# Kernel tuning notes

Measured on AMD Instinct MI355X. Metric: run time of the kernel, lower is better.

The kernel has to match this reference:

```python
import jax, jax.numpy as jnp
import numpy as np

# Module config (matches init_kwargs)
B, H, W, C = 8, 32, 32, 512
NH = 8                      # num_heads
D = C // NH                 # per-head qkv channels (downsize_factor = num_heads)
HO = 512 // NH              # head_output_channels = output_channels // num_heads
COUT = 512                  # output_channels (== C so shortcut works)
EPS = 1e-3                  # keras BatchNormalization default epsilon


def setup_inputs() -> dict:
    key = jax.random.key(0)
    ks = jax.random.split(key, 10)
    s_in = C ** -0.5
    return {
        "x": jax.random.normal(ks[0], (B, H, W, C), jnp.float32),
        # 1x1 convs == per-head matmuls, no bias (use_bias=False)
        "Wk": jax.random.normal(ks[1], (NH, C, D), jnp.float32) * s_in,
        "Wq": jax.random.normal(ks[2], (NH, C, D), jnp.float32) * s_in,
        "Wv": jax.random.normal(ks[3], (NH, C, D), jnp.float32) * s_in,
        "Wo_head": jax.random.normal(ks[4], (NH, D, HO), jnp.float32) * (D ** -0.5),
        # per-head BatchNorm (inference: moving statistics)
        "gamma": jnp.ones((NH, HO), jnp.float32),
        "beta": jnp.zeros((NH, HO), jnp.float32),
        "mov_mean": jnp.zeros((NH, HO), jnp.float32),
        "mov_var": jnp.ones((NH, HO), jnp.float32),
        # relative position embeddings, init stddev = channels**-0.5
        "rel_w": jax.random.normal(ks[5], (NH, 2 * W - 1, D), jnp.float32) * s_in,
        "rel_h": jax.random.normal(ks[6], (NH, 2 * H - 1, D), jnp.float32) * s_in,
        # final 1x1 conv over concatenated heads
        "Wout": jax.random.normal(ks[7], (NH * HO, COUT), jnp.float32) * ((NH * HO) ** -0.5),
    }


def rel_to_abs(x):
    # x: [b, nh, L, 2L-1] relative logits -> [b, nh, L, L] absolute logits
    b, nh, L, _ = x.shape
    x = jnp.pad(x, ((0, 0), (0, 0), (0, 0), (0, 1)))        # [b,nh,L,2L]
    flat = x.reshape(b, nh, L * 2 * L)
    flat = jnp.pad(flat, ((0, 0), (0, 0), (0, L - 1)))       # [b,nh,2L^2+L-1]
    final = flat.reshape(b, nh, L + 1, 2 * L - 1)
    return final[:, :, :L, L - 1:]


def reference(x, Wk, Wq, Wv, Wo_head, gamma, beta, mov_mean, mov_var, rel_w, rel_h, Wout):
    b, h, w, c = x.shape
    n = h * w
    xf = x.reshape(b, n, c)
    # per-head 1x1 conv projections -> [b, nh, n, d]
    k = jnp.einsum('bnc,hcd->bhnd', xf, Wk)
    q = jnp.einsum('bnc,hcd->bhnd', xf, Wq)
    v = jnp.einsum('bnc,hcd->bhnd', xf, Wv)
    # Keras Dot(axes=2)([key, query]): rows index key positions, cols query positions
    scores = jnp.einsum('bhid,bhjd->bhij', k, q)             # [b,nh,n,n]
    # relative position logits computed from q (spatial mode)
    q5 = q.reshape(b, NH, h, w, D)
    wl = jnp.einsum('bhxyd,hmd->bhxym', q5, rel_w)           # [b,nh,H,W,2W-1]
    w_abs = rel_to_abs(wl.reshape(b * NH, h, w, 2 * w - 1)).reshape(b, NH, h, w, w)
    hl = jnp.einsum('bhxyd,hmd->bhyxm', q5, rel_h)           # [b,nh,W,H,2H-1] (q transposed x<->y)
    h_abs = rel_to_abs(hl.reshape(b * NH, w, h, 2 * h - 1)).reshape(b, NH, w, h, h)
    h_abs = h_abs.transpose(0, 1, 3, 2, 4)                   # [b,nh,x,y,x2]
    # logits[(x,y),(x2,y2)] = w_abs[x,y,y2] + h_abs[x,y,x2]
    s6 = scores.reshape(b, NH, h, w, h, w)
    s6 = s6 + w_abs[:, :, :, :, None, :] + h_abs[:, :, :, :, :, None]
    attn = jax.nn.softmax(s6.reshape(b, NH, n, n), axis=-1)
    out = jnp.einsum('bhij,bhjd->bhid', attn, v)             # [b,nh,n,d]
    ho = jnp.einsum('bhid,hde->bhie', out, Wo_head)          # per-head output 1x1 conv
    # per-head BatchNorm (inference)
    ho = gamma[None, :, None, :] * (ho - mov_mean[None, :, None, :]) * \
         jax.lax.rsqrt(mov_var[None, :, None, :] + EPS) + beta[None, :, None, :]
    cat = ho.transpose(0, 2, 1, 3).reshape(b, n, NH * HO)    # channel concat of heads
    y = (cat @ Wout).reshape(b, h, w, COUT)                  # final 1x1 conv
    return y + x                                             # shortcut connection
```

## Files before the change

### kernel.cpp

```cpp
#include <hip/hip_runtime.h>
#include <stdint.h>

typedef unsigned short u16;
typedef __attribute__((ext_vector_type(8))) short short8;
typedef __attribute__((ext_vector_type(4))) float f32x4;
typedef __attribute__((ext_vector_type(16))) float f32x16;
typedef __attribute__((ext_vector_type(4))) unsigned short us4;
typedef __attribute__((ext_vector_type(4))) uint32_t u32x4;
typedef __attribute__((ext_vector_type(2))) int i32x2;
typedef __attribute__((ext_vector_type(4))) int i32x4;

#define MFMA(a,b,c)   __builtin_amdgcn_mfma_f32_16x16x32_bf16((a),(b),(c),0,0,0)
#define MFMA32(a,b,c) __builtin_amdgcn_mfma_f32_32x32x16_bf16((a),(b),(c),0,0,0)
#define L2E 1.44269504f

__device__ __forceinline__ u16 f2bf(float f){
    union { float f; uint32_t i; } v; v.f = f;
    uint32_t u = v.i;
    return (u16)((u + 0x7fffu + ((u >> 16) & 1u)) >> 16);
}
__device__ __forceinline__ uint32_t cvtpk(float lo, float hi){
    uint32_t r;
    asm("v_cvt_pk_bf16_f32 %0, %1, %2" : "=v"(r) : "v"(lo), "v"(hi));
    return r;
}
__device__ __forceinline__ void barrier_lgkm(){
    __builtin_amdgcn_sched_barrier(0);
    asm volatile("s_waitcnt lgkmcnt(0)" ::: "memory");
    __builtin_amdgcn_s_barrier();
    __builtin_amdgcn_sched_barrier(0);
}

#define WS_W1T    0u
#define WS_WOT    1572864u
#define WS_WOUTT  1638400u
#define WS_RELW   2162688u
#define WS_RELH   2227200u
#define WS_SCALE  2291712u
#define WS_SHIFT  2293760u
#define WS_Q      10684416u
#define WS_K      19073024u
#define WS_VT     27461632u
#define WS_Z      52627456u

__global__ __launch_bounds__(256) void k0_setup(
    const float* Wk, const float* Wq, const float* Wv, const float* Wo,
    const float* gamma, const float* beta, const float* mean, const float* var,
    const float* relw, const float* relh, const float* Wout,
    u16* W1T, u16* WoT, u16* WoutT,
    u16* RWbf, u16* RHbf, float* scaleZ, float* shiftZ)
{
    int idx = blockIdx.x * 256 + threadIdx.x;
    if (idx < 786432) {
        int co = idx >> 9, c = idx & 511;
        int p = co >> 9, rem = co & 511;
        int h = rem >> 6, d = rem & 63;
        const float* src = (p == 0) ? Wq : (p == 1) ? Wk : Wv;
        W1T[idx] = f2bf(src[h * 32768 + c * 64 + d]);
    } else if (idx < 819200) {
        int r = idx - 786432;
        int h = r >> 12; int e = (r & 4095) >> 6, ep = r & 63;
        WoT[h * 4096 + ep * 64 + e] = f2bf(Wo[h * 4096 + e * 64 + ep]);
    } else if (idx < 1081344) {
        int r = idx - 819200;
        int c = r >> 9, co = r & 511;
        WoutT[co * 512 + c] = f2bf(Wout[c * 512 + co]);
    } else if (idx < 1145856) {
        int r = idx - 1081344;
        if (r < 32256) RWbf[r] = f2bf(relw[r]);
        else           RHbf[r - 32256] = f2bf(relh[r - 32256]);
    } else if (idx < 1146368) {
        int ch = idx - 1145856;
        float sc = gamma[ch] * rsqrtf(var[ch] + 1e-3f);
        scaleZ[ch] = sc;
        shiftZ[ch] = beta[ch] - mean[ch] * sc;
    }
}

__device__ __forceinline__ void packA(u16* dst, f32x4 a0, f32x4 a1, f32x4 a2, f32x4 a3){
    u32x4 v0 = { cvtpk(a0.x,a0.y), cvtpk(a0.z,a0.w), cvtpk(a1.x,a1.y), cvtpk(a1.z,a1.w) };
    u32x4 v1 = { cvtpk(a2.x,a2.y), cvtpk(a2.z,a2.w), cvtpk(a3.x,a3.y), cvtpk(a3.z,a3.w) };
    *(u32x4*)dst = v0;
    *(u32x4*)(dst + 8) = v1;
}

__global__ __launch_bounds__(256, 3) void k1_gemm(
    const float* __restrict__ Xf, const u16* __restrict__ W1T,
    u16* Q, u16* K, u16* Vt)
{
    int s = blockIdx.x;
    int xcd = s & 7, r8 = s >> 3;
    int nt = r8 % 12, mt = (r8 / 12) * 8 + xcd;
    int tid = threadIdx.x;
    int w = tid >> 6, l = tid & 63, lg = l >> 4, ll = l & 15;
    int wm = w >> 1, wn = w & 1;
    int i0 = mt * 128, co0 = nt * 128;

    __shared__ __align__(16) u16 SM[20480];
    u16* As = SM;
    u16* Bs = SM + 10240;

    int row = tid >> 1, c16 = (tid & 1) * 16;
    int st = row * 40 + c16;
    const float* ArowF = Xf + (size_t)(i0 + row) * 512 + c16;
    const u16*   Brow  = W1T + (size_t)(co0 + row) * 512 + c16;

    f32x4 acc[4][4];
#pragma unroll
    for (int m = 0; m < 4; m++)
#pragma unroll
        for (int nn = 0; nn < 4; nn++) acc[m][nn] = (f32x4){0,0,0,0};

    f32x4 ra0 = *(const f32x4*)&ArowF[0];
    f32x4 ra1 = *(const f32x4*)&ArowF[4];
    f32x4 ra2 = *(const f32x4*)&ArowF[8];
    f32x4 ra3 = *(const f32x4*)&ArowF[12];
    short8 rb0 = *(const short8*)&Brow[0];
    short8 rb1 = *(const short8*)&Brow[8];
    packA(&As[st], ra0, ra1, ra2, ra3);
    *(short8*)&Bs[st] = rb0; *(short8*)&Bs[st + 8] = rb1;
    __syncthreads();
    for (int ks = 0; ks < 16; ++ks) {
        int cur = ks & 1, nxt = cur ^ 1;
        if (ks < 15) {
            ra0 = *(const f32x4*)&ArowF[(ks + 1) * 32];
            ra1 = *(const f32x4*)&ArowF[(ks + 1) * 32 + 4];
            ra2 = *(const f32x4*)&ArowF[(ks + 1) * 32 + 8];
            ra3 = *(const f32x4*)&ArowF[(ks + 1) * 32 + 12];
            rb0 = *(const short8*)&Brow[(ks + 1) * 32];
            rb1 = *(const short8*)&Brow[(ks + 1) * 32 + 8];
        }
        const u16* Ab = As + cur * 5120;
        const u16* Bb = Bs + cur * 5120;
        short8 af[4], bfr[4];
#pragma unroll
        for (int m = 0; m < 4; m++)
            af[m] = *(const short8*)&Ab[(wm * 64 + m * 16 + ll) * 40 + lg * 8];
#pragma unroll
        for (int nn = 0; nn < 4; nn++)
            bfr[nn] = *(const short8*)&Bb[(wn * 64 + nn * 16 + ll) * 40 + lg * 8];
#pragma unroll
        for (int m = 0; m < 4; m++)
#pragma unroll
            for (int nn = 0; nn < 4; nn++)
                acc[m][nn] = MFMA(af[m], bfr[nn], acc[m][nn]);
        if (ks < 15) {
            int so = nxt * 5120 + st;
            packA(&As[so], ra0, ra1, ra2, ra3);
            *(short8*)&Bs[so] = rb0; *(short8*)&Bs[so + 8] = rb1;
        }
        __syncthreads();
    }

    int b = mt >> 3, nloc0 = (mt & 7) * 128;
    u16* Ts = SM;
    if (nt < 8) {
        u16* dst = (nt < 4) ? Q : K;
        float qsc = (nt < 4) ? L2E : 1.0f;
        int coB = (nt & 3) * 128;
#pragma unroll
        for (int nn = 0; nn < 4; nn++)
#pragma unroll
            for (int m = 0; m < 4; m++)
#pragma unroll
                for (int r = 0; r < 4; r++)
                    Ts[(wm * 64 + m * 16 + lg * 4 + r) * 136 + wn * 64 + nn * 16 + ll]
                        = f2bf(acc[m][nn][r] * qsc);
        __syncthreads();
        int chunk = tid & 7;
#pragma unroll
        for (int j = 0; j < 8; j++) {
            int vr = j * 32 + (tid >> 3);
            int irow = vr >> 1, half = vr & 1;
            int hh = (coB >> 6) + half;
            u16* qdst = dst + ((size_t)(b * 8 + hh) * 1024 + nloc0 + irow) * 64;
            *(short8*)&qdst[chunk * 8] = *(const short8*)&Ts[irow * 136 + half * 64 + chunk * 8];
        }
    } else {
#pragma unroll
        for (int nn = 0; nn < 4; nn++)
#pragma unroll
            for (int m = 0; m < 4; m++)
#pragma unroll
                for (int r = 0; r < 4; r++)
                    Ts[(wn * 64 + nn * 16 + ll) * 136 + wm * 64 + m * 16 + lg * 4 + r]
                        = f2bf(acc[m][nn][r]);
        __syncthreads();
        int co_l = tid >> 1, half = tid & 1;
        int co = (nt - 8) * 128 + co_l;
        int hh = (co >> 6) & 7, d = co & 63;
        u16* vdst = Vt + ((size_t)(b * 8 + hh) * 64 + d) * 1024 + nloc0 + half * 64;
#pragma unroll
        for (int j = 0; j < 8; j++)
            *(short8*)&vdst[j * 8] = *(const short8*)&Ts[co_l * 136 + half * 64 + j * 8];
    }
}

__global__ __launch_bounds__(256, 2) void k2_attn(
    const u16* Q, const u16* K, const u16* Vt,
    const u16* relwb, const u16* relhb,
    const u16* WoT, const float* scaleZ, const float* shiftZ,
    u16* Z)
{
    int s_ = blockIdx.x;
    int xcd = s_ & 7, r8 = s_ >> 3;
    int it = r8 & 7, bh = (r8 >> 3) * 8 + xcd;
    int b = bh >> 3, h = bh & 7;
    int tid = threadIdx.x;
    int wv = tid >> 6, l = tid & 63, il = l & 31, hf = l >> 5;
    int i0 = it * 128;
    int iw = i0 + wv * 32;

    __shared__ __align__(16) char smem[53760];
    u16*   Qs  = (u16*)smem;
    u16*   Vs  = (u16*)(smem + 18432);
    float* rhS = (float*)(smem + 36864);

    const u16* kb = K + ((size_t)bh * 1024 + iw) * 64;
    short8 kf0 = *(const short8*)&kb[il * 64 + hf * 8];
    short8 kf1 = *(const short8*)&kb[il * 64 + 16 + hf * 8];
    short8 kf2 = *(const short8*)&kb[il * 64 + 32 + hf * 8];
    short8 kf3 = *(const short8*)&kb[il * 64 + 48 + hf * 8];

    float rw16[16];
    {
        float* wlb = (float*)(smem + wv * 8448);
        const u16* qsrc = Q + ((size_t)bh * 1024 + iw) * 64;
        short8 qa0 = *(const short8*)&qsrc[il * 64 + hf * 8];
        short8 qa1 = *(const short8*)&qsrc[il * 64 + 16 + hf * 8];
        short8 qa2 = *(const short8*)&qsrc[il * 64 + 32 + hf * 8];
        short8 qa3 = *(const short8*)&qsrc[il * 64 + 48 + hf * 8];
        int m1 = (32 + il > 62) ? 62 : 32 + il;
        const u16* rwsrc = relwb + h * 4032;
        const u16* rhsrc = relhb + h * 4032;
#pragma unroll
        for (int mt2 = 0; mt2 < 2; mt2++) {
            int m = mt2 ? m1 : il;
            short8 b0 = *(const short8*)&rwsrc[m * 64 + hf * 8];
            short8 b1 = *(const short8*)&rwsrc[m * 64 + 16 + hf * 8];
            short8 b2 = *(const short8*)&rwsrc[m * 64 + 32 + hf * 8];
            short8 b3 = *(const short8*)&rwsrc[m * 64 + 48 + hf * 8];
            f32x16 wa;
#pragma unroll
            for (int reg = 0; reg < 16; reg++) wa[reg] = 0.f;
            wa = MFMA32(qa0, b0, wa);
            wa = MFMA32(qa1, b1, wa);
            wa = MFMA32(qa2, b2, wa);
            wa = MFMA32(qa3, b3, wa);
#pragma unroll
            for (int reg = 0; reg < 16; reg++)
                wlb[((reg & 3) + 8 * (reg >> 2) + 4 * hf) * 66 + mt2 * 32 + il] = wa[reg];
        }
#pragma unroll
        for (int reg = 0; reg < 16; reg++) {
            int c = (reg & 3) + 8 * (reg >> 2) + 4 * hf;
            rw16[reg] = wlb[il * 65 + c + 31];
        }
#pragma unroll
        for (int mt2 = 0; mt2 < 2; mt2++) {
            int m = mt2 ? m1 : il;
            short8 b0 = *(const short8*)&rhsrc[m * 64 + hf * 8];
            short8 b1 = *(const short8*)&rhsrc[m * 64 + 16 + hf * 8];
            short8 b2 = *(const short8*)&rhsrc[m * 64 + 32 + hf * 8];
            short8 b3 = *(const short8*)&rhsrc[m * 64 + 48 + hf * 8];
            f32x16 ha;
#pragma unroll
            for (int reg = 0; reg < 16; reg++) ha[reg] = 0.f;
            ha = MFMA32(qa0, b0, ha);
            ha = MFMA32(qa1, b1, ha);
            ha = MFMA32(qa2, b2, ha);
            ha = MFMA32(qa3, b3, ha);
#pragma unroll
            for (int reg = 0; reg < 16; reg++)
                wlb[((reg & 3) + 8 * (reg >> 2) + 4 * hf) * 66 + mt2 * 32 + il] = ha[reg];
        }
        int x = iw >> 5;
#pragma unroll
        for (int reg = 0; reg < 16; reg++) {
            int c = (reg & 3) + 8 * (reg >> 2) + 4 * hf;
            rhS[(wv * 32 + il) * 33 + c] = wlb[il * 66 + c + 31 - x];
        }
    }
    __syncthreads();

    f32x16 o0, o1;
#pragma unroll
    for (int reg = 0; reg < 16; reg++) { o0[reg] = 0.f; o1[reg] = 0.f; }
    float lsum = 0.f;

    const u16* qg = Q + (size_t)bh * 65536;
    const u16* vg = Vt + (size_t)bh * 65536;
    int srow = tid >> 2, sg = (tid & 3) * 8;

    short8 pq0 = *(const short8*)&qg[(size_t)srow * 64 + sg];
    short8 pq1 = *(const short8*)&qg[(size_t)srow * 64 + sg + 32];
    short8 pv0 = *(const short8*)&vg[(size_t)srow * 1024 + sg];
    short8 pv1 = *(const short8*)&vg[(size_t)srow * 1024 + sg + 32];
    *(short8*)&Qs[srow * 72 + sg] = pq0;
    *(short8*)&Qs[srow * 72 + sg + 32] = pq1;
    *(short8*)&Vs[srow * 72 + sg] = pv0;
    *(short8*)&Vs[srow * 72 + sg + 32] = pv1;
    pq0 = *(const short8*)&qg[(size_t)(64 + srow) * 64 + sg];
    pq1 = *(const short8*)&qg[(size_t)(64 + srow) * 64 + sg + 32];
    pv0 = *(const short8*)&vg[(size_t)srow * 1024 + 64 + sg];
    pv1 = *(const short8*)&vg[(size_t)srow * 1024 + 64 + sg + 32];

    for (int ch = 0; ch < 16; ++ch) {
        int cur = ch & 1, nxt = cur ^ 1;
        barrier_lgkm();
        if (ch < 15) {
            *(short8*)&Qs[nxt * 4608 + srow * 72 + sg] = pq0;
            *(short8*)&Qs[nxt * 4608 + srow * 72 + sg + 32] = pq1;
            *(short8*)&Vs[nxt * 4608 + srow * 72 + sg] = pv0;
            *(short8*)&Vs[nxt * 4608 + srow * 72 + sg + 32] = pv1;
        }
        if (ch < 14) {
            int j2 = (ch + 2) * 64;
            pq0 = *(const short8*)&qg[(size_t)(j2 + srow) * 64 + sg];
            pq1 = *(const short8*)&qg[(size_t)(j2 + srow) * 64 + sg + 32];
            pv0 = *(const short8*)&vg[(size_t)srow * 1024 + j2 + sg];
            pv1 = *(const short8*)&vg[(size_t)srow * 1024 + j2 + sg + 32];
        }
        const u16* Qb = Qs + cur * 4608;
        const u16* Vb = Vs + cur * 4608;

#pragma unroll
        for (int u = 0; u < 2; ++u) {
            int jl = u * 32;
            float rhv = rhS[(wv * 32 + il) * 33 + ch * 2 + u];
            f32x16 sA;
#pragma unroll
            for (int reg = 0; reg < 16; reg++) sA[reg] = rw16[reg] + rhv;
            short8 aq0 = *(const short8*)&Qb[(jl + il) * 72 + hf * 8];
            short8 aq1 = *(const short8*)&Qb[(jl + il) * 72 + 16 + hf * 8];
            short8 aq2 = *(const short8*)&Qb[(jl + il) * 72 + 32 + hf * 8];
            short8 aq3 = *(const short8*)&Qb[(jl + il) * 72 + 48 + hf * 8];
            sA = MFMA32(aq0, kf0, sA);
            sA = MFMA32(aq1, kf1, sA);
            sA = MFMA32(aq2, kf2, sA);
            sA = MFMA32(aq3, kf3, sA);

            float p[16];
#pragma unroll
            for (int reg = 0; reg < 16; reg++) p[reg] = __builtin_amdgcn_exp2f(sA[reg]);
            {
                float t0 = (p[0] + p[1]) + (p[2] + p[3]);
                float t1 = (p[4] + p[5]) + (p[6] + p[7]);
                float t2 = (p[8] + p[9]) + (p[10] + p[11]);
                float t3 = (p[12] + p[13]) + (p[14] + p[15]);
                lsum += (t0 + t1) + (t2 + t3);
            }
            uint32_t W[8];
#pragma unroll
            for (int q = 0; q < 4; q++) {
                W[q * 2]     = cvtpk(p[q * 4 + 0], p[q * 4 + 1]);
                W[q * 2 + 1] = cvtpk(p[q * 4 + 2], p[q * 4 + 3]);
            }
            short8 pf0, pf1;
            {
                i32x2 rA = __builtin_amdgcn_permlane32_swap((int)W[0], (int)W[2], false, false);
                i32x2 rB = __builtin_amdgcn_permlane32_swap((int)W[1], (int)W[3], false, false);
                i32x4 t = { rA.x, rB.x, rA.y, rB.y };
                pf0 = *(short8*)&t;
            }
            {
                i32x2 rA = __builtin_amdgcn_permlane32_swap((int)W[4], (int)W[6], false, false);
                i32x2 rB = __builtin_amdgcn_permlane32_swap((int)W[5], (int)W[7], false, false);
                i32x4 t = { rA.x, rB.x, rA.y, rB.y };
                pf1 = *(short8*)&t;
            }

            __builtin_amdgcn_s_setprio(1);
            short8 av;
            av = *(const short8*)&Vb[il * 72 + jl + hf * 8];
            o0 = MFMA32(av, pf0, o0);
            av = *(const short8*)&Vb[(32 + il) * 72 + jl + hf * 8];
            o1 = MFMA32(av, pf0, o1);
            av = *(const short8*)&Vb[il * 72 + jl + 16 + hf * 8];
            o0 = MFMA32(av, pf1, o0);
            av = *(const short8*)&Vb[(32 + il) * 72 + jl + 16 + hf * 8];
            o1 = MFMA32(av, pf1, o1);
            __builtin_amdgcn_s_setprio(0);
        }
    }

    lsum += __shfl_xor(lsum, 32);
    float inv = 1.0f / lsum;
    __syncthreads();

    u16* Ob = (u16*)smem + wv * 2304;
#pragma unroll
    for (int q = 0; q < 4; q++) {
        uint32_t w0 = cvtpk(o0[q * 4 + 0] * inv, o0[q * 4 + 1] * inv);
        uint32_t w1 = cvtpk(o0[q * 4 + 2] * inv, o0[q * 4 + 3] * inv);
        *(uint32_t*)&Ob[il * 72 + q * 8 + hf * 4]     = w0;
        *(uint32_t*)&Ob[il * 72 + q * 8 + hf * 4 + 2] = w1;
        uint32_t w2 = cvtpk(o1[q * 4 + 0] * inv, o1[q * 4 + 1] * inv);
        uint32_t w3 = cvtpk(o1[q * 4 + 2] * inv, o1[q * 4 + 3] * inv);
        *(uint32_t*)&Ob[il * 72 + 32 + q * 8 + hf * 4]     = w2;
        *(uint32_t*)&Ob[il * 72 + 32 + q * 8 + hf * 4 + 2] = w3;
    }
    short8 ao0 = *(const short8*)&Ob[il * 72 + hf * 8];
    short8 ao1 = *(const short8*)&Ob[il * 72 + 16 + hf * 8];
    short8 ao2 = *(const short8*)&Ob[il * 72 + 32 + hf * 8];
    short8 ao3 = *(const short8*)&Ob[il * 72 + 48 + hf * 8];

    const u16* wob = WoT + h * 4096;
#pragma unroll
    for (int et = 0; et < 2; et++) {
        short8 bo0 = *(const short8*)&wob[(et * 32 + il) * 64 + hf * 8];
        short8 bo1 = *(const short8*)&wob[(et * 32 + il) * 64 + 16 + hf * 8];
        short8 bo2 = *(const short8*)&wob[(et * 32 + il) * 64 + 32 + hf * 8];
        short8 bo3 = *(const short8*)&wob[(et * 32 + il) * 64 + 48 + hf * 8];
        f32x16 zacc;
#pragma unroll
        for (int reg = 0; reg < 16; reg++) zacc[reg] = 0.f;
        zacc = MFMA32(ao0, bo0, zacc);
        zacc = MFMA32(ao1, bo1, zacc);
        zacc = MFMA32(ao2, bo2, zacc);
        zacc = MFMA32(ao3, bo3, zacc);
        int chn = h * 64 + et * 32 + il;
        float scv = scaleZ[chn], shv = shiftZ[chn];
#pragma unroll
        for (int reg = 0; reg < 16; reg++) {
            int i = iw + (reg & 3) + 8 * (reg >> 2) + 4 * hf;
            Z[((size_t)(b * 1024) + i) * 512 + chn] = f2bf(zacc[reg] * scv + shv);
        }
    }
}

__global__ __launch_bounds__(256, 4) void k3_gemm(
    const u16* __restrict__ Zb, const u16* __restrict__ WoutT,
    const float* __restrict__ X, float* Y)
{
    int s = blockIdx.x;
    int xcd = s & 7, r8 = s >> 3;
    int nt = r8 & 7, mt = (r8 >> 3) * 8 + xcd;
    int tid = threadIdx.x;
    int w = tid >> 6, l = tid & 63, lg = l >> 4, ll = l & 15;
    int wm = w >> 1, wn = w & 1;
    int i0 = mt * 64, co0 = nt * 64;

    __shared__ __align__(16) u16 SM[10240];
    u16* As = SM;
    u16* Bs = SM + 5120;

    int row = tid >> 2, c8 = (tid & 3) * 8;
    int st = row * 40 + c8;
    const u16* Arow = Zb + (size_t)(i0 + row) * 512 + c8;
    const u16* Brow = WoutT + (size_t)(co0 + row) * 512 + c8;

    f32x4 acc[2][2];
#pragma unroll
    for (int m = 0; m < 2; m++)
#pragma unroll
        for (int nn = 0; nn < 2; nn++) acc[m][nn] = (f32x4){0,0,0,0};

    short8 ra = *(const short8*)&Arow[0];
    short8 rb = *(const short8*)&Brow[0];
    *(short8*)&As[st] = ra;
    *(short8*)&Bs[st] = rb;
    __syncthreads();
    for (int ks = 0; ks < 16; ++ks) {
        int cur = ks & 1, nxt = cur ^ 1;
        if (ks < 15) {
            ra = *(const short8*)&Arow[(ks + 1) * 32];
            rb = *(const short8*)&Brow[(ks + 1) * 32];
        }
        const u16* Ab = As + cur * 2560;
        const u16* Bb = Bs + cur * 2560;
        short8 af[2], bfr[2];
#pragma unroll
        for (int m = 0; m < 2; m++)
            af[m] = *(const short8*)&Ab[(wm * 32 + m * 16 + ll) * 40 + lg * 8];
#pragma unroll
        for (int nn = 0; nn < 2; nn++)
            bfr[nn] = *(const short8*)&Bb[(wn * 32 + nn * 16 + ll) * 40 + lg * 8];
#pragma unroll
        for (int m = 0; m < 2; m++)
#pragma unroll
            for (int nn = 0; nn < 2; nn++)
                acc[m][nn] = MFMA(af[m], bfr[nn], acc[m][nn]);
        if (ks < 15) {
            int so = nxt * 2560 + st;
            *(short8*)&As[so] = ra;
            *(short8*)&Bs[so] = rb;
        }
        __syncthreads();
    }

#pragma unroll
    for (int m = 0; m < 2; m++)
#pragma unroll
        for (int nn = 0; nn < 2; nn++) {
            int i = i0 + wm * 32 + m * 16 + lg * 4;
            int co = co0 + wn * 32 + nn * 16 + ll;
#pragma unroll
            for (int r = 0; r < 4; r++) {
                size_t idx = (size_t)(i + r) * 512 + co;
                Y[idx] = acc[m][nn][r] + X[idx];
            }
        }
}

extern "C" void kernel_launch(void* const* d_in, const int* in_sizes, int n_in,
                              void* d_out, int out_size, void* d_ws, size_t ws_size,
                              hipStream_t stream)
{
    const float* x     = (const float*)d_in[0];
    const float* Wk    = (const float*)d_in[1];
    const float* Wq    = (const float*)d_in[2];
    const float* Wv    = (const float*)d_in[3];
    const float* Wo    = (const float*)d_in[4];
    const float* gamma = (const float*)d_in[5];
    const float* beta  = (const float*)d_in[6];
    const float* mmean = (const float*)d_in[7];
    const float* mvar  = (const float*)d_in[8];
    const float* relw  = (const float*)d_in[9];
    const float* relh  = (const float*)d_in[10];
    const float* Wout  = (const float*)d_in[11];

    char* ws = (char*)d_ws;
    u16*   W1T    = (u16*)(ws + WS_W1T);
    u16*   WoT    = (u16*)(ws + WS_WOT);
    u16*   WoutT  = (u16*)(ws + WS_WOUTT);
    u16*   RWbf   = (u16*)(ws + WS_RELW);
    u16*   RHbf   = (u16*)(ws + WS_RELH);
    float* scaleZ = (float*)(ws + WS_SCALE);
    float* shiftZ = (float*)(ws + WS_SHIFT);
    u16*   Qw     = (u16*)(ws + WS_Q);
    u16*   Kw     = (u16*)(ws + WS_K);
    u16*   Vtw    = (u16*)(ws + WS_VT);
    u16*   Zw     = (u16*)(ws + WS_Z);

    k0_setup<<<4478, 256, 0, stream>>>(Wk, Wq, Wv, Wo, gamma, beta, mmean, mvar,
                                       relw, relh, Wout,
                                       W1T, WoT, WoutT, RWbf, RHbf,
                                       scaleZ, shiftZ);
    k1_gemm<<<768, 256, 0, stream>>>(x, W1T, Qw, Kw, Vtw);
    k2_attn<<<512, 256, 0, stream>>>(Qw, Kw, Vtw, RWbf, RHbf, WoT, scaleZ, shiftZ, Zw);
    k3_gemm<<<1024, 256, 0, stream>>>(Zw, WoutT, x, (float*)d_out);
}
```

Before: 85.59 us.

## Load GEMM operand fragments directly from global memory, bypassing LDS staging

In the QKV projection GEMM the weight operand is now read from global memory straight into MFMA fragment registers with one-step register prefetch, instead of going through a double-buffered LDS tile. Only the activation tile stays in LDS, and the barrier becomes an LDS-only wait. The output-projection GEMM drops LDS entirely and reads both operands directly from global memory, with the k-loop fully unrolled. This removes LDS traffic and barriers but relies on L1/L2 to absorb the duplicated and less coalesced global reads, and it raises register pressure.

```diff
diff --git a/kernel.cpp b/kernel.cpp
--- a/kernel.cpp
+++ b/kernel.cpp
@@ -98,12 +98,11 @@
 
     __shared__ __align__(16) u16 SM[20480];
     u16* As = SM;
-    u16* Bs = SM + 10240;
 
     int row = tid >> 1, c16 = (tid & 1) * 16;
     int st = row * 40 + c16;
     const float* ArowF = Xf + (size_t)(i0 + row) * 512 + c16;
-    const u16*   Brow  = W1T + (size_t)(co0 + row) * 512 + c16;
+    const u16*   Bg    = W1T + (size_t)(co0 + wn * 64 + ll) * 512 + lg * 8;
 
     f32x4 acc[4][4];
 #pragma unroll
@@ -115,11 +114,13 @@
     f32x4 ra1 = *(const f32x4*)&ArowF[4];
     f32x4 ra2 = *(const f32x4*)&ArowF[8];
     f32x4 ra3 = *(const f32x4*)&ArowF[12];
-    short8 rb0 = *(const short8*)&Brow[0];
-    short8 rb1 = *(const short8*)&Brow[8];
+    short8 bnxt[4];
+#pragma unroll
+    for (int nn = 0; nn < 4; nn++)
+        bnxt[nn] = *(const short8*)&Bg[nn * 8192];
     packA(&As[st], ra0, ra1, ra2, ra3);
-    *(short8*)&Bs[st] = rb0; *(short8*)&Bs[st + 8] = rb1;
     __syncthreads();
+#pragma unroll
     for (int ks = 0; ks < 16; ++ks) {
         int cur = ks & 1, nxt = cur ^ 1;
         if (ks < 15) {
@@ -127,29 +128,27 @@
             ra1 = *(const f32x4*)&ArowF[(ks + 1) * 32 + 4];
             ra2 = *(const f32x4*)&ArowF[(ks + 1) * 32 + 8];
             ra3 = *(const f32x4*)&ArowF[(ks + 1) * 32 + 12];
-            rb0 = *(const short8*)&Brow[(ks + 1) * 32];
-            rb1 = *(const short8*)&Brow[(ks + 1) * 32 + 8];
+        }
+        short8 bcur[4];
+#pragma unroll
+        for (int nn = 0; nn < 4; nn++) bcur[nn] = bnxt[nn];
+        if (ks < 15) {
+#pragma unroll
+            for (int nn = 0; nn < 4; nn++)
+                bnxt[nn] = *(const short8*)&Bg[nn * 8192 + (ks + 1) * 32];
         }
         const u16* Ab = As + cur * 5120;
-        const u16* Bb = Bs + cur * 5120;
-        short8 af[4], bfr[4];
+        short8 af[4];
 #pragma unroll
         for (int m = 0; m < 4; m++)
             af[m] = *(const short8*)&Ab[(wm * 64 + m * 16 + ll) * 40 + lg * 8];
 #pragma unroll
-        for (int nn = 0; nn < 4; nn++)
-            bfr[nn] = *(const short8*)&Bb[(wn * 64 + nn * 16 + ll) * 40 + lg * 8];
-#pragma unroll
         for (int m = 0; m < 4; m++)
 #pragma unroll
             for (int nn = 0; nn < 4; nn++)
-                acc[m][nn] = MFMA(af[m], bfr[nn], acc[m][nn]);
-        if (ks < 15) {
-            int so = nxt * 5120 + st;
-            packA(&As[so], ra0, ra1, ra2, ra3);
-            *(short8*)&Bs[so] = rb0; *(short8*)&Bs[so + 8] = rb1;
-        }
-        __syncthreads();
+                acc[m][nn] = MFMA(af[m], bcur[nn], acc[m][nn]);
+        if (ks < 15) packA(&As[nxt * 5120 + st], ra0, ra1, ra2, ra3);
+        barrier_lgkm();
     }
 
     int b = mt >> 3, nloc0 = (mt & 7) * 128;
@@ -441,14 +440,8 @@
     int wm = w >> 1, wn = w & 1;
     int i0 = mt * 64, co0 = nt * 64;
 
-    __shared__ __align__(16) u16 SM[10240];
-    u16* As = SM;
-    u16* Bs = SM + 5120;
-
-    int row = tid >> 2, c8 = (tid & 3) * 8;
-    int st = row * 40 + c8;
-    const u16* Arow = Zb + (size_t)(i0 + row) * 512 + c8;
-    const u16* Brow = WoutT + (size_t)(co0 + row) * 512 + c8;
+    const u16* Ag = Zb    + (size_t)(i0 + wm * 32 + ll) * 512 + lg * 8;
+    const u16* Bg = WoutT + (size_t)(co0 + wn * 32 + ll) * 512 + lg * 8;
 
     f32x4 acc[2][2];
 #pragma unroll
@@ -456,37 +449,20 @@
 #pragma unroll
         for (int nn = 0; nn < 2; nn++) acc[m][nn] = (f32x4){0,0,0,0};
 
-    short8 ra = *(const short8*)&Arow[0];
-    short8 rb = *(const short8*)&Brow[0];
-    *(short8*)&As[st] = ra;
-    *(short8*)&Bs[st] = rb;
-    __syncthreads();
+#pragma unroll
     for (int ks = 0; ks < 16; ++ks) {
-        int cur = ks & 1, nxt = cur ^ 1;
-        if (ks < 15) {
-            ra = *(const short8*)&Arow[(ks + 1) * 32];
-            rb = *(const short8*)&Brow[(ks + 1) * 32];
-        }
-        const u16* Ab = As + cur * 2560;
-        const u16* Bb = Bs + cur * 2560;
         short8 af[2], bfr[2];
 #pragma unroll
         for (int m = 0; m < 2; m++)
-            af[m] = *(const short8*)&Ab[(wm * 32 + m * 16 + ll) * 40 + lg * 8];
+            af[m] = *(const short8*)&Ag[m * 16 * 512 + ks * 32];
 #pragma unroll
         for (int nn = 0; nn < 2; nn++)
-            bfr[nn] = *(const short8*)&Bb[(wn * 32 + nn * 16 + ll) * 40 + lg * 8];
+            bfr[nn] = *(const short8*)&Bg[nn * 16 * 512 + ks * 32];
 #pragma unroll
         for (int m = 0; m < 2; m++)
 #pragma unroll
             for (int nn = 0; nn < 2; nn++)
                 acc[m][nn] = MFMA(af[m], bfr[nn], acc[m][nn]);
-        if (ks < 15) {
-            int so = nxt * 2560 + st;
-            *(short8*)&As[so] = ra;
-            *(short8*)&Bs[so] = rb;
-        }
-        __syncthreads();
     }
 
 #pragma unroll
```

Result: slower. 111.9 us (+30.8%).
